# Performance work log

Measured on AMD Instinct MI355X. Metric: run time of the kernel, lower is better.

Reference implementation:

```python
import jax, jax.numpy as jnp
import numpy as np

BS, V, H, W = 2, 4, 24, 24
C, K, L, NH = 256, 16, 6, 8
DH = C // NH
FF = 4 * C
EPS = 1e-5


def _ln(x, w, b):
    m = jnp.mean(x, axis=-1, keepdims=True)
    v = jnp.mean((x - m) ** 2, axis=-1, keepdims=True)
    return (x - m) * jax.lax.rsqrt(v + EPS) * w + b


def _pe(x, W1, b1, W2, b2):
    # PositionEmbeddingLearnedMLP: Linear(3,C) -> ReLU -> Linear(C,C), channels-last
    return jax.nn.relu(x @ W1.T + b1) @ W2.T + b2


def setup_inputs():
    key = jax.random.key(0)
    ks = jax.random.split(key, 8)
    s = 0.02
    return {
        "feature": jax.random.normal(ks[0], (BS * V, C, H, W), jnp.float32),
        "xyz": jax.random.uniform(ks[1], (BS * V, H, W, 3), jnp.float32),
        "pe_W1": jax.random.normal(ks[2], (C, 3), jnp.float32) * s,
        "pe_b1": jnp.zeros((C,), jnp.float32),
        "pe_W2": jax.random.normal(ks[3], (C, C), jnp.float32) * s,
        "pe_b2": jnp.zeros((C,), jnp.float32),
        "Wqkv": jax.random.normal(ks[4], (L, 3 * C, C), jnp.float32) * s,
        "bqkv": jnp.zeros((L, 3 * C), jnp.float32),
        "Wo": jax.random.normal(ks[5], (L, C, C), jnp.float32) * s,
        "bo": jnp.zeros((L, C), jnp.float32),
        "ln_attn_w": jnp.ones((L, C), jnp.float32),
        "ln_attn_b": jnp.zeros((L, C), jnp.float32),
        "W1": jax.random.normal(ks[6], (L, FF, C), jnp.float32) * s,
        "b1": jnp.zeros((L, FF), jnp.float32),
        "W2": jax.random.normal(ks[7], (L, C, FF), jnp.float32) * s,
        "b2": jnp.zeros((L, C), jnp.float32),
        "ln_ffn_w": jnp.ones((L, C), jnp.float32),
        "ln_ffn_b": jnp.zeros((L, C), jnp.float32),
        "ln_out_w": jnp.ones((L, C), jnp.float32),
        "ln_out_b": jnp.zeros((L, C), jnp.float32),
    }


def _forward(feature, xyz, pe_W1, pe_b1, pe_W2, pe_b2, Wqkv, bqkv, Wo, bo,
             ln_attn_w, ln_attn_b, W1, b1, W2, b2, ln_ffn_w, ln_ffn_b,
             ln_out_w, ln_out_b):
    N = V * H * W
    # (B*V,C,H,W) -> (BS,N,C) ; (B*V,H,W,3) -> (BS,N,3) : flatten views+pixels
    feat = feature.reshape(BS, V, C, H, W).transpose(0, 1, 3, 4, 2).reshape(BS, N, C)
    pts = xyz.reshape(BS, N, 3)
    # per-batch KNN (self included), mirroring pointops.queryandgroup
    d2 = jnp.sum((pts[:, :, None, :] - pts[:, None, :, :]) ** 2, axis=-1)  # (BS,N,N)
    _, idx = jax.lax.top_k(-d2, K)  # (BS,N,K) nearest-neighbor indices
    grouped = jax.vmap(lambda p, i: p[i])(pts, idx)  # (BS,N,K,3)
    rel = grouped - pts[:, :, None, :]  # relative coords (use_xyz=True)
    q_pe = _pe(jnp.zeros((3,), feat.dtype), pe_W1, pe_b1, pe_W2, pe_b2)  # (C,)
    k_pe = _pe(rel, pe_W1, pe_b1, pe_W2, pe_b2).reshape(BS * N, K, C)
    idx_g = (idx + (jnp.arange(BS) * N)[:, None, None]).reshape(BS * N, K)
    out = feat.reshape(BS * N, C)
    for i in range(L):
        keyf = out[idx_g]  # (BN,K,C) per-layer neighbor gather
        # CrossAttentionLayer, pre-norm
        t2 = _ln(out, ln_attn_w[i], ln_attn_b[i])
        q = (t2 + q_pe) @ Wqkv[i, :C].T + bqkv[i, :C]
        k = (keyf + k_pe) @ Wqkv[i, C:2 * C].T + bqkv[i, C:2 * C]
        v = keyf @ Wqkv[i, 2 * C:].T + bqkv[i, 2 * C:]
        qh = q.reshape(-1, NH, DH)
        kh = k.reshape(-1, K, NH, DH)
        vh = v.reshape(-1, K, NH, DH)
        att = jax.nn.softmax(jnp.einsum('bhd,bkhd->bhk', qh, kh) * (DH ** -0.5), axis=-1)
        ao = jnp.einsum('bhk,bkhd->bhd', att, vh).reshape(-1, C) @ Wo[i].T + bo[i]
        out = out + ao
        # FFNLayer, pre-norm
        t2 = _ln(out, ln_ffn_w[i], ln_ffn_b[i])
        out = out + (jax.nn.relu(t2 @ W1[i].T + b1[i]) @ W2[i].T + b2[i])
        # extra per-layer LayerNorm
        out = _ln(out, ln_out_w[i], ln_out_b[i])
    return out.reshape(BS, V, H, W, C).transpose(0, 1, 4, 2, 3).reshape(BS * V, C, H, W)


def reference(feature, xyz, pe_W1, pe_b1, pe_W2, pe_b2, Wqkv, bqkv, Wo, bo,
              ln_attn_w, ln_attn_b, W1, b1, W2, b2, ln_ffn_w, ln_ffn_b,
              ln_out_w, ln_out_b):
    return _forward(feature, xyz, pe_W1, pe_b1, pe_W2, pe_b2, Wqkv, bqkv, Wo, bo,
                    ln_attn_w, ln_attn_b, W1, b1, W2, b2, ln_ffn_w, ln_ffn_b,
                    ln_out_w, ln_out_b)
```

## Files before the change

### kernel.cpp

```cpp
#include <hip/hip_runtime.h>
#include <math.h>

#define BS_ 2
#define V_ 4
#define H_ 24
#define W_ 24
#define N_ (V_*H_*W_)
#define BN_ (BS_*N_)
#define C_ 256
#define K_ 16
#define L_ 6
#define NH_ 8
#define DH_ 32
#define FF_ 1024

typedef __attribute__((ext_vector_type(4))) float f32x4;
typedef __attribute__((ext_vector_type(8))) short bf16x8;
typedef __attribute__((ext_vector_type(4))) unsigned u32x4;

__device__ inline unsigned short f2bf(float x) {
    unsigned u = __float_as_uint(x);
    unsigned r = u + 0x7fffu + ((u >> 16) & 1u);
    return (unsigned short)(r >> 16);
}
__device__ inline float bf2f(unsigned short h) {
    return __uint_as_float(((unsigned)h) << 16);
}

__global__ __launch_bounds__(256) void f2bf_kernel(const float* __restrict__ in,
                                                   unsigned short* __restrict__ out, int n) {
    int i = blockIdx.x*256 + threadIdx.x;
    if (i < n) out[i] = f2bf(in[i]);
}

__global__ __launch_bounds__(256) void w2frag_kernel(const float* __restrict__ W,
                                                     unsigned short* __restrict__ F,
                                                     int P, int K) {
    int wid = threadIdx.x >> 6, lane = threadIdx.x & 63;
    int tile = blockIdx.x*4 + wid;
    int nkt = K >> 5;
    int tn = tile / nkt, tk = tile - tn*nkt;
    const float* src = W + (size_t)(tn*16 + (lane & 15))*K + tk*32 + (lane >> 4)*8;
    unsigned short tmp[8];
    #pragma unroll
    for (int j = 0; j < 8; ++j) tmp[j] = f2bf(src[j]);
    *(bf16x8*)&F[(size_t)tile*512 + lane*8] = *(bf16x8*)tmp;
}

__global__ __launch_bounds__(256) void reshape_in_ln(const float* __restrict__ f,
                                                     const float* __restrict__ lnw,
                                                     const float* __restrict__ lnb,
                                                     const float* __restrict__ qpe,
                                                     float* __restrict__ w_out,
                                                     unsigned short* __restrict__ b_out,
                                                     unsigned short* __restrict__ b_t2) {
    int bn = blockIdx.x, c = threadIdx.x;
    int b = bn / N_, rem = bn % N_;
    int v = rem / (H_*W_), hw = rem % (H_*W_);
    float x = f[(((size_t)(b*V_ + v)*C_ + c)*(H_*W_)) + hw];
    w_out[(size_t)bn*C_ + c] = x;
    b_out[(size_t)bn*C_ + c] = f2bf(x);
    __shared__ float red[4];
    float s = x;
    #pragma unroll
    for (int off = 32; off; off >>= 1) s += __shfl_xor(s, off, 64);
    if ((c & 63) == 0) red[c >> 6] = s;
    __syncthreads();
    float mean = (red[0]+red[1]+red[2]+red[3]) * (1.f/C_);
    __syncthreads();
    float dx = x - mean;
    s = dx*dx;
    #pragma unroll
    for (int off = 32; off; off >>= 1) s += __shfl_xor(s, off, 64);
    if ((c & 63) == 0) red[c >> 6] = s;
    __syncthreads();
    float var = (red[0]+red[1]+red[2]+red[3]) * (1.f/C_);
    float y = dx * rsqrtf(var + 1e-5f) * lnw[c] + lnb[c] + qpe[c];
    b_t2[(size_t)bn*C_ + c] = f2bf(y);
}

__global__ __launch_bounds__(256) void reshape_out_kernel(const float* __restrict__ in,
                                                          float* __restrict__ o) {
    int bn = blockIdx.x, c = threadIdx.x;
    int b = bn / N_, rem = bn % N_;
    int v = rem / (H_*W_), hw = rem % (H_*W_);
    o[(((size_t)(b*V_ + v)*C_ + c)*(H_*W_)) + hw] = in[(size_t)bn*C_ + c];
}

__global__ __launch_bounds__(256) void knn_kernel(const float* __restrict__ pts,
                                                  int* __restrict__ idx) {
    int wid = threadIdx.x >> 6, lane = threadIdx.x & 63;
    int point = blockIdx.x*4 + wid;
    int b = point / N_;
    int il = point % N_;
    __shared__ float ps[N_*3];
    for (int l = threadIdx.x; l < N_*3; l += 256) ps[l] = pts[(size_t)b*N_*3 + l];
    __syncthreads();
    float qx = ps[il*3], qy = ps[il*3+1], qz = ps[il*3+2];
    unsigned long long key[36];
    #pragma unroll
    for (int s = 0; s < 36; ++s) {
        int j = lane + 64*s;
        float dx = qx - ps[j*3], dy = qy - ps[j*3+1], dz = qz - ps[j*3+2];
        float d2 = dx*dx + dy*dy + dz*dz;
        key[s] = ((unsigned long long)__float_as_uint(d2) << 32) | (unsigned)j;
    }
    for (int it = 0; it < K_; ++it) {
        unsigned long long b0 = key[0], b1 = key[1], b2 = key[2], b3 = key[3];
        #pragma unroll
        for (int s = 4; s < 36; s += 4) {
            b0 = key[s]   < b0 ? key[s]   : b0;
            b1 = key[s+1] < b1 ? key[s+1] : b1;
            b2 = key[s+2] < b2 ? key[s+2] : b2;
            b3 = key[s+3] < b3 ? key[s+3] : b3;
        }
        unsigned long long m01 = b0 < b1 ? b0 : b1;
        unsigned long long m23 = b2 < b3 ? b2 : b3;
        unsigned long long best = m01 < m23 ? m01 : m23;
        #pragma unroll
        for (int off = 32; off; off >>= 1) {
            unsigned long long o = __shfl_xor(best, off, 64);
            if (o < best) best = o;
        }
        int wj = (int)(best & 0xffffffffu);
        if (lane == 0) idx[point*K_ + it] = b*N_ + wj;
        if ((wj & 63) == lane) {
            int sw = wj >> 6;
            #pragma unroll
            for (int s = 0; s < 36; ++s) if (s == sw) key[s] = ~0ull;
        }
    }
}

__global__ __launch_bounds__(256) void qpe_kernel(const float* __restrict__ b1,
                                                  const float* __restrict__ W2,
                                                  const float* __restrict__ b2,
                                                  float* __restrict__ qpe) {
    __shared__ float h[C_];
    int tid = threadIdx.x;
    h[tid] = fmaxf(b1[tid], 0.f);
    __syncthreads();
    float acc = 0.f;
    for (int j = 0; j < C_; ++j) acc += h[j] * W2[(size_t)tid*C_ + j];
    qpe[tid] = acc + b2[tid];
}

__global__ __launch_bounds__(256) void pe_hidden_kernel(const float* __restrict__ pts,
                                                        const int* __restrict__ idx,
                                                        const float* __restrict__ W1,
                                                        const float* __restrict__ b1,
                                                        unsigned short* __restrict__ hidden) {
    int point = blockIdx.x;
    int c = threadIdx.x;
    __shared__ float rel[K_][3];
    if (threadIdx.x < K_*3) {
        int k = threadIdx.x / 3, ax = threadIdx.x % 3;
        int j = idx[point*K_ + k];
        rel[k][ax] = pts[(size_t)j*3 + ax] - pts[(size_t)point*3 + ax];
    }
    __syncthreads();
    float w0 = W1[c*3], w1 = W1[c*3+1], w2 = W1[c*3+2], bb = b1[c];
    #pragma unroll
    for (int k = 0; k < K_; ++k) {
        float v = rel[k][0]*w0 + rel[k][1]*w1 + rel[k][2]*w2 + bb;
        hidden[((size_t)point*K_ + k)*C_ + c] = f2bf(fmaxf(v, 0.f));
    }
}

template<int ACT, bool RES, int OMODE>
__device__ __forceinline__ void gemm_body2(const unsigned short* __restrict__ A, int sA,
                                           const unsigned short* __restrict__ Wf,
                                           const float* __restrict__ bias, int bcol0,
                                           const float* __restrict__ res,
                                           float* __restrict__ outF,
                                           unsigned short* __restrict__ outB,
                                           int sO, int on0, int m0, int K) {
    __shared__ unsigned short As[2][64][40];
    int tid = threadIdx.x;
    int wave = tid >> 6, lane = tid & 63;
    int wr = wave >> 1, wc = wave & 1;
    int nkt = K >> 5;
    f32x4 acc[2][2];
    #pragma unroll
    for (int i = 0; i < 2; ++i)
        #pragma unroll
        for (int j = 0; j < 2; ++j) acc[i][j] = (f32x4){0.f, 0.f, 0.f, 0.f};

    int r = tid >> 2, ch = tid & 3;
    const unsigned short* pA = A + (size_t)(m0 + r)*sA + ch*8;
    const unsigned short* bb = Wf + (size_t)(wc*2)*nkt*512 + lane*8;
    *(bf16x8*)&As[0][r][ch*8] = *(const bf16x8*)pA;
    bf16x8 bw0 = *(const bf16x8*)bb;
    bf16x8 bw1 = *(const bf16x8*)(bb + (size_t)nkt*512);
    __syncthreads();
    for (int t = 0; t < nkt; ++t) {
        int cur = t & 1;
        bool nx = (t + 1 < nkt);
        bf16x8 la, nb0, nb1;
        if (nx) {
            la  = *(const bf16x8*)(pA + (t+1)*32);
            nb0 = *(const bf16x8*)(bb + (size_t)(t+1)*512);
            nb1 = *(const bf16x8*)(bb + (size_t)nkt*512 + (size_t)(t+1)*512);
        }
        int kf = (lane >> 4) * 8;
        bf16x8 af0 = *(const bf16x8*)&As[cur][wr*32 + (lane & 15)][kf];
        bf16x8 af1 = *(const bf16x8*)&As[cur][wr*32 + 16 + (lane & 15)][kf];
        acc[0][0] = __builtin_amdgcn_mfma_f32_16x16x32_bf16(af0, bw0, acc[0][0], 0, 0, 0);
        acc[0][1] = __builtin_amdgcn_mfma_f32_16x16x32_bf16(af0, bw1, acc[0][1], 0, 0, 0);
        acc[1][0] = __builtin_amdgcn_mfma_f32_16x16x32_bf16(af1, bw0, acc[1][0], 0, 0, 0);
        acc[1][1] = __builtin_amdgcn_mfma_f32_16x16x32_bf16(af1, bw1, acc[1][1], 0, 0, 0);
        if (nx) *(bf16x8*)&As[cur^1][r][ch*8] = la;
        bw0 = nb0; bw1 = nb1;
        __syncthreads();
    }
    #pragma unroll
    for (int i = 0; i < 2; ++i) {
        #pragma unroll
        for (int j = 0; j < 2; ++j) {
            #pragma unroll
            for (int rg = 0; rg < 4; ++rg) {
                int m = m0 + wr*32 + i*16 + (lane >> 4)*4 + rg;
                int pl = wc*32 + j*16 + (lane & 15);
                float v = acc[i][j][rg];
                if (bias) v += bias[bcol0 + pl];
                if (ACT == 1) v = fmaxf(v, 0.f);
                if (RES) v += res[(size_t)m*sO + on0 + pl];
                if (OMODE != 2) outF[(size_t)m*sO + on0 + pl] = v;
                if (OMODE != 0) outB[(size_t)m*sO + on0 + pl] = f2bf(v);
            }
        }
    }
}

template<int ACT, bool RES, int OMODE>
__global__ __launch_bounds__(256) void gemm_k2(const unsigned short* __restrict__ A,
                                               const unsigned short* __restrict__ Wf0,
                                               const float* __restrict__ bias,
                                               const float* __restrict__ res,
                                               float* __restrict__ outF,
                                               unsigned short* __restrict__ outB,
                                               int P, int K) {
    int n0 = blockIdx.x * 64, m0 = blockIdx.y * 64;
    const unsigned short* Wf = Wf0 + (size_t)(n0 >> 4)*(K >> 5)*512;
    gemm_body2<ACT,RES,OMODE>(A, K, Wf, bias, n0, res, outF, outB, P, n0, m0, K);
}

__global__ __launch_bounds__(256) void qkv_kernel2(const unsigned short* __restrict__ t2,
                                                   const unsigned short* __restrict__ outb,
                                                   const unsigned short* __restrict__ Fqkv_l,
                                                   const float* __restrict__ bqkv_l,
                                                   unsigned short* __restrict__ b_q,
                                                   unsigned short* __restrict__ b_kv) {
    int bx = blockIdx.x;
    int m0 = blockIdx.y * 64;
    const unsigned short* Wf = Fqkv_l + (size_t)(bx*4)*8*512;
    if (bx < 4) {
        gemm_body2<0,false,2>(t2, C_, Wf, bqkv_l, bx*64, nullptr, nullptr, b_q, 256, bx*64, m0, C_);
    } else {
        gemm_body2<0,false,2>(outb, C_, Wf, bqkv_l, bx*64, nullptr, nullptr, b_kv, 512, bx*64 - 256, m0, C_);
    }
}

template<int VAR>
__global__ __launch_bounds__(256) void gemm_ln2(const unsigned short* __restrict__ A,
                                                const unsigned short* __restrict__ Wf,
                                                const float* __restrict__ bias,
                                                const float* __restrict__ res,
                                                const float* __restrict__ lnw1, const float* __restrict__ lnb1,
                                                const float* __restrict__ lnw2, const float* __restrict__ lnb2,
                                                const float* __restrict__ qpe,
                                                float* __restrict__ outF,
                                                unsigned short* __restrict__ outB,
                                                unsigned short* __restrict__ outT2,
                                                int K) {
    __shared__ unsigned short As[2][16][40];
    __shared__ float S[16][260];
    int tid = threadIdx.x;
    int wave = tid >> 6, lane = tid & 63;
    int m0 = blockIdx.x * 16;
    int nkt = K >> 5;
    f32x4 acc[4];
    #pragma unroll
    for (int j = 0; j < 4; ++j) acc[j] = (f32x4){0.f,0.f,0.f,0.f};
    const unsigned short* pA = A + (size_t)(m0 + ((tid & 63) >> 2))*K + (tid & 3)*8;
    const unsigned short* bb = Wf + (size_t)(wave*4)*nkt*512 + lane*8;
    if (tid < 64) *(bf16x8*)&As[0][tid >> 2][(tid & 3)*8] = *(const bf16x8*)pA;
    bf16x8 bw[4];
    #pragma unroll
    for (int j = 0; j < 4; ++j) bw[j] = *(const bf16x8*)(bb + (size_t)j*nkt*512);
    __syncthreads();
    for (int t = 0; t < nkt; ++t) {
        int cur = t & 1;
        bool nx = (t + 1 < nkt);
        bf16x8 la, nb0, nb1, nb2, nb3;
        if (nx) {
            nb0 = *(const bf16x8*)(bb + (size_t)0*nkt*512 + (size_t)(t+1)*512);
            nb1 = *(const bf16x8*)(bb + (size_t)1*nkt*512 + (size_t)(t+1)*512);
            nb2 = *(const bf16x8*)(bb + (size_t)2*nkt*512 + (size_t)(t+1)*512);
            nb3 = *(const bf16x8*)(bb + (size_t)3*nkt*512 + (size_t)(t+1)*512);
            if (tid < 64) la = *(const bf16x8*)(pA + (t+1)*32);
        }
        int kf = (lane >> 4) * 8;
        bf16x8 af = *(const bf16x8*)&As[cur][lane & 15][kf];
        acc[0] = __builtin_amdgcn_mfma_f32_16x16x32_bf16(af, bw[0], acc[0], 0, 0, 0);
        acc[1] = __builtin_amdgcn_mfma_f32_16x16x32_bf16(af, bw[1], acc[1], 0, 0, 0);
        acc[2] = __builtin_amdgcn_mfma_f32_16x16x32_bf16(af, bw[2], acc[2], 0, 0, 0);
        acc[3] = __builtin_amdgcn_mfma_f32_16x16x32_bf16(af, bw[3], acc[3], 0, 0, 0);
        if (nx) {
            if (tid < 64) *(bf16x8*)&As[cur^1][tid >> 2][(tid & 3)*8] = la;
            bw[0] = nb0; bw[1] = nb1; bw[2] = nb2; bw[3] = nb3;
        }
        __syncthreads();
    }
    #pragma unroll
    for (int j = 0; j < 4; ++j) {
        int col = wave*64 + j*16 + (lane & 15);
        #pragma unroll
        for (int rg = 0; rg < 4; ++rg) {
            int row = (lane >> 4)*4 + rg;
            S[row][col] = acc[j][rg] + bias[col] + res[(size_t)(m0+row)*C_ + col];
        }
    }
    __syncthreads();
    int row = tid >> 4, g = tid & 15;
    size_t m = m0 + row;
    float x[16];
    #pragma unroll
    for (int u = 0; u < 4; ++u) {
        f32x4 v4 = *(const f32x4*)&S[row][g*16 + u*4];
        x[u*4+0] = v4[0]; x[u*4+1] = v4[1]; x[u*4+2] = v4[2]; x[u*4+3] = v4[3];
    }
    float s1 = 0.f, s2 = 0.f;
    #pragma unroll
    for (int u = 0; u < 16; ++u) { s1 += x[u]; s2 += x[u]*x[u]; }
    #pragma unroll
    for (int off = 8; off; off >>= 1) { s1 += __shfl_xor(s1, off, 16); s2 += __shfl_xor(s2, off, 16); }
    float mean = s1 * (1.f/C_);
    float var  = s2 * (1.f/C_) - mean*mean;
    float rstd = rsqrtf(var + 1e-5f);
    float y1[16];
    #pragma unroll
    for (int u = 0; u < 4; ++u) {
        f32x4 w4 = *(const f32x4*)&lnw1[g*16 + u*4];
        f32x4 b4 = *(const f32x4*)&lnb1[g*16 + u*4];
        #pragma unroll
        for (int v = 0; v < 4; ++v)
            y1[u*4+v] = (x[u*4+v] - mean)*rstd*w4[v] + b4[v];
    }
    if (VAR == 0) {
        #pragma unroll
        for (int u = 0; u < 4; ++u) {
            f32x4 v4 = { x[u*4], x[u*4+1], x[u*4+2], x[u*4+3] };
            *(f32x4*)&outF[m*C_ + g*16 + u*4] = v4;
        }
        unsigned pk[8];
        #pragma unroll
        for (int u = 0; u < 8; ++u) pk[u] = (unsigned)f2bf(y1[2*u]) | ((unsigned)f2bf(y1[2*u+1]) << 16);
        *(u32x4*)&outT2[m*C_ + g*16]     = *(u32x4*)&pk[0];
        *(u32x4*)&outT2[m*C_ + g*16 + 8] = *(u32x4*)&pk[4];
    } else {
        #pragma unroll
        for (int u = 0; u < 4; ++u) {
            f32x4 v4 = { y1[u*4], y1[u*4+1], y1[u*4+2], y1[u*4+3] };
            *(f32x4*)&outF[m*C_ + g*16 + u*4] = v4;
        }
        if (VAR == 1) {
            unsigned pk[8];
            #pragma unroll
            for (int u = 0; u < 8; ++u) pk[u] = (unsigned)f2bf(y1[2*u]) | ((unsigned)f2bf(y1[2*u+1]) << 16);
            *(u32x4*)&outB[m*C_ + g*16]     = *(u32x4*)&pk[0];
            *(u32x4*)&outB[m*C_ + g*16 + 8] = *(u32x4*)&pk[4];
            float t1 = 0.f, t2s = 0.f;
            #pragma unroll
            for (int u = 0; u < 16; ++u) { t1 += y1[u]; t2s += y1[u]*y1[u]; }
            #pragma unroll
            for (int off = 8; off; off >>= 1) { t1 += __shfl_xor(t1, off, 16); t2s += __shfl_xor(t2s, off, 16); }
            float mean2 = t1 * (1.f/C_);
            float var2  = t2s * (1.f/C_) - mean2*mean2;
            float rstd2 = rsqrtf(var2 + 1e-5f);
            unsigned pk2[8];
            #pragma unroll
            for (int u = 0; u < 4; ++u) {
                f32x4 w4 = *(const f32x4*)&lnw2[g*16 + u*4];
                f32x4 b4 = *(const f32x4*)&lnb2[g*16 + u*4];
                f32x4 q4 = *(const f32x4*)&qpe[g*16 + u*4];
                float z0 = (y1[u*4+0]-mean2)*rstd2*w4[0] + b4[0] + q4[0];
                float z1 = (y1[u*4+1]-mean2)*rstd2*w4[1] + b4[1] + q4[1];
                float z2 = (y1[u*4+2]-mean2)*rstd2*w4[2] + b4[2] + q4[2];
                float z3 = (y1[u*4+3]-mean2)*rstd2*w4[3] + b4[3] + q4[3];
                pk2[u*2]   = (unsigned)f2bf(z0) | ((unsigned)f2bf(z1) << 16);
                pk2[u*2+1] = (unsigned)f2bf(z2) | ((unsigned)f2bf(z3) << 16);
            }
            *(u32x4*)&outT2[m*C_ + g*16]     = *(u32x4*)&pk2[0];
            *(u32x4*)&outT2[m*C_ + g*16 + 8] = *(u32x4*)&pk2[4];
        }
    }
}

__global__ __launch_bounds__(256) void rk_kernel(const unsigned short* __restrict__ q,
                                                 const unsigned short* __restrict__ Wqkv_l,
                                                 unsigned short* __restrict__ r) {
    int n0 = blockIdx.x * 64, m0 = blockIdx.y * 64, h = blockIdx.z;
    __shared__ unsigned short As[64][40];
    __shared__ unsigned short Ws[64][40];
    int tid = threadIdx.x;
    int wave = tid >> 6, lane = tid & 63;
    int wr = wave >> 1, wc = wave & 1;
    *(bf16x8*)&As[tid>>2][(tid&3)*8] =
        *(const bf16x8*)&q[(size_t)(m0 + (tid>>2))*C_ + h*DH_ + (tid&3)*8];
    {
        int d = tid >> 3, cg = tid & 7;
        bf16x8 wv = *(const bf16x8*)&Wqkv_l[(size_t)(C_ + h*DH_ + d)*C_ + n0 + cg*8];
        #pragma unroll
        for (int j = 0; j < 8; ++j) Ws[cg*8 + j][d] = (unsigned short)wv[j];
    }
    __syncthreads();
    int kf = (lane >> 4) * 8;
    bf16x8 af[2], wf[2];
    #pragma unroll
    for (int i = 0; i < 2; ++i) af[i] = *(const bf16x8*)&As[wr*32 + i*16 + (lane & 15)][kf];
    #pragma unroll
    for (int j = 0; j < 2; ++j) wf[j] = *(const bf16x8*)&Ws[wc*32 + j*16 + (lane & 15)][kf];
    f32x4 acc[2][2];
    #pragma unroll
    for (int i = 0; i < 2; ++i)
        #pragma unroll
        for (int j = 0; j < 2; ++j)
            acc[i][j] = __builtin_amdgcn_mfma_f32_16x16x32_bf16(af[i], wf[j],
                          (f32x4){0.f,0.f,0.f,0.f}, 0, 0, 0);
    #pragma unroll
    for (int i = 0; i < 2; ++i)
        #pragma unroll
        for (int j = 0; j < 2; ++j)
            #pragma unroll
            for (int rg = 0; rg < 4; ++rg) {
                int m = m0 + wr*32 + i*16 + (lane >> 4)*4 + rg;
                int pl = wc*32 + j*16 + (lane & 15);
                r[(size_t)m*(NH_*C_) + h*C_ + n0 + pl] = f2bf(acc[i][j][rg]);
            }
}

__global__ __launch_bounds__(256) void attn_kernel(const unsigned short* __restrict__ q,
                                                   const unsigned short* __restrict__ kv,
                                                   const unsigned short* __restrict__ kpe,
                                                   const unsigned short* __restrict__ r,
                                                   const int* __restrict__ idx,
                                                   unsigned short* __restrict__ ao) {
    int wid = threadIdx.x >> 6, lane = threadIdx.x & 63;
    int point = blockIdx.x*4 + wid;
    __shared__ __align__(16) unsigned short vs[4][K_][264];
    __shared__ __align__(16) float atts[4][NH_][K_];
    int row = lane & 15;
    int off8 = (lane >> 4) * 8;
    int idx_l = idx[point*K_ + row];

    #pragma unroll
    for (int t = 0; t < 8; ++t) {
        int vr = 2*t + (lane >> 5);
        int j = __shfl(idx_l, vr, 64);
        int cc = (lane & 31) * 8;
        *(bf16x8*)&vs[wid][vr][cc] = *(const bf16x8*)&kv[(size_t)j*512 + 256 + cc];
    }

    f32x4 acc = {0.f, 0.f, 0.f, 0.f};
    const bf16x8 zero8 = {0,0,0,0,0,0,0,0};
    #pragma unroll
    for (int s = 0; s < 8; ++s) {
        bf16x8 a = *(const bf16x8*)&kpe[((size_t)point*K_ + row)*C_ + s*32 + off8];
        bf16x8 b = zero8;
        if (row < 8) b = *(const bf16x8*)&r[(size_t)point*NH_*C_ + row*C_ + s*32 + off8];
        acc = __builtin_amdgcn_mfma_f32_16x16x32_bf16(a, b, acc, 0, 0, 0);
    }
    #pragma unroll
    for (int s = 0; s < 8; ++s) {
        bf16x8 a = *(const bf16x8*)&kv[(size_t)idx_l*512 + s*32 + off8];
        bf16x8 b = zero8;
        if (row == 8 + s) b = *(const bf16x8*)&q[(size_t)point*C_ + s*32 + off8];
        acc = __builtin_amdgcn_mfma_f32_16x16x32_bf16(a, b, acc, 0, 0, 0);
    }

    const float scale = 0.1767766952966369f;
    float sv[4], m = -1e30f;
    #pragma unroll
    for (int rg = 0; rg < 4; ++rg) {
        float o = __shfl_xor(acc[rg], 8, 64);
        sv[rg] = (acc[rg] + o) * scale;
        m = fmaxf(m, sv[rg]);
    }
    m = fmaxf(m, __shfl_xor(m, 16, 64));
    m = fmaxf(m, __shfl_xor(m, 32, 64));
    float sum = 0.f;
    #pragma unroll
    for (int rg = 0; rg < 4; ++rg) { sv[rg] = __expf(sv[rg] - m); sum += sv[rg]; }
    sum += __shfl_xor(sum, 16, 64);
    sum += __shfl_xor(sum, 32, 64);
    float inv = 1.f / sum;
    if (row < 8) {
        f32x4 av = { sv[0]*inv, sv[1]*inv, sv[2]*inv, sv[3]*inv };
        *(f32x4*)&atts[wid][row][(lane >> 4) * 4] = av;
    }

    int h = lane >> 3;
    float att_f[16];
    #pragma unroll
    for (int u = 0; u < 4; ++u) {
        f32x4 t4 = *(const f32x4*)&atts[wid][h][u*4];
        att_f[u*4+0] = t4[0]; att_f[u*4+1] = t4[1]; att_f[u*4+2] = t4[2]; att_f[u*4+3] = t4[3];
    }
    int cbase = lane * 4;
    float o0 = 0.f, o1 = 0.f, o2 = 0.f, o3 = 0.f;
    #pragma unroll
    for (int k = 0; k < K_; ++k) {
        unsigned long long vv = *(const unsigned long long*)&vs[wid][k][cbase];
        unsigned lo = (unsigned)vv, hi = (unsigned)(vv >> 32);
        float a = att_f[k];
        o0 += a * __uint_as_float(lo << 16);
        o1 += a * __uint_as_float(lo & 0xffff0000u);
        o2 += a * __uint_as_float(hi << 16);
        o3 += a * __uint_as_float(hi & 0xffff0000u);
    }
    unsigned p0 = (unsigned)f2bf(o0) | ((unsigned)f2bf(o1) << 16);
    unsigned p1 = (unsigned)f2bf(o2) | ((unsigned)f2bf(o3) << 16);
    unsigned out2[2] = { p0, p1 };
    *(unsigned long long*)&ao[(size_t)point*C_ + cbase] = *(const unsigned long long*)out2;
}

extern "C" void kernel_launch(void* const* d_in, const int* in_sizes, int n_in,
                              void* d_out, int out_size, void* d_ws, size_t ws_size,
                              hipStream_t stream) {
    const float* feature  = (const float*)d_in[0];
    const float* xyz      = (const float*)d_in[1];
    const float* pe_W1    = (const float*)d_in[2];
    const float* pe_b1    = (const float*)d_in[3];
    const float* pe_W2    = (const float*)d_in[4];
    const float* pe_b2    = (const float*)d_in[5];
    const float* Wqkv     = (const float*)d_in[6];
    const float* bqkv     = (const float*)d_in[7];
    const float* Wo       = (const float*)d_in[8];
    const float* bo       = (const float*)d_in[9];
    const float* ln_attn_w= (const float*)d_in[10];
    const float* ln_attn_b= (const float*)d_in[11];
    const float* W1       = (const float*)d_in[12];
    const float* b1       = (const float*)d_in[13];
    const float* W2       = (const float*)d_in[14];
    const float* b2       = (const float*)d_in[15];
    const float* ln_ffn_w = (const float*)d_in[16];
    const float* ln_ffn_b = (const float*)d_in[17];
    const float* ln_out_w = (const float*)d_in[18];
    const float* ln_out_b = (const float*)d_in[19];

    float* ws = (float*)d_ws;
    float* w_out = ws;
    float* w_qpe = w_out + (size_t)BN_*C_;
    unsigned short* bptr = (unsigned short*)(w_qpe + C_ + 64);
    unsigned short* b_out = bptr;  bptr += (size_t)BN_*C_;
    unsigned short* b_t2  = bptr;  bptr += (size_t)BN_*C_;
    unsigned short* b_q   = bptr;  bptr += (size_t)BN_*C_;
    unsigned short* b_kv  = bptr;  bptr += (size_t)BN_*512;
    unsigned short* b_ao  = bptr;  bptr += (size_t)BN_*C_;
    unsigned short* b_ffh = bptr;  bptr += (size_t)BN_*FF_;
    unsigned short* w_kpe = bptr;  bptr += (size_t)BN_*K_*C_;
    unsigned short* w_r   = bptr;  bptr += (size_t)BN_*NH_*C_;
    unsigned short* b_hid = bptr;  bptr += (size_t)BN_*K_*C_;
    unsigned short* bWqkv = bptr;  bptr += (size_t)L_*3*C_*C_;
    unsigned short* Fqkv  = bptr;  bptr += (size_t)L_*3*C_*C_;
    unsigned short* Fo    = bptr;  bptr += (size_t)L_*C_*C_;
    unsigned short* F1    = bptr;  bptr += (size_t)L_*FF_*C_;
    unsigned short* F2    = bptr;  bptr += (size_t)L_*C_*FF_;
    unsigned short* Fpe   = bptr;  bptr += (size_t)C_*C_;
    int* w_idx = (int*)bptr;

    f2bf_kernel<<<(L_*3*C_*C_+255)/256, 256, 0, stream>>>(Wqkv, bWqkv, L_*3*C_*C_);
    w2frag_kernel<<<(L_*3*C_*C_/512)/4, 256, 0, stream>>>(Wqkv, Fqkv, L_*3*C_, C_);
    w2frag_kernel<<<(L_*C_*C_/512)/4,   256, 0, stream>>>(Wo,   Fo,   L_*C_,   C_);
    w2frag_kernel<<<(L_*FF_*C_/512)/4,  256, 0, stream>>>(W1,   F1,   L_*FF_,  C_);
    w2frag_kernel<<<(L_*C_*FF_/512)/4,  256, 0, stream>>>(W2,   F2,   L_*C_,   FF_);
    w2frag_kernel<<<(C_*C_/512)/4,      256, 0, stream>>>(pe_W2, Fpe, C_,      C_);

    knn_kernel<<<BN_/4, 256, 0, stream>>>(xyz, w_idx);
    qpe_kernel<<<1, 256, 0, stream>>>(pe_b1, pe_W2, pe_b2, w_qpe);
    reshape_in_ln<<<BN_, 256, 0, stream>>>(feature, ln_attn_w, ln_attn_b, w_qpe,
                                           w_out, b_out, b_t2);
    pe_hidden_kernel<<<BN_, 256, 0, stream>>>(xyz, w_idx, pe_W1, pe_b1, b_hid);
    gemm_k2<0,false,2><<<dim3(C_/64, (BN_*K_)/64), 256, 0, stream>>>(
        b_hid, Fpe, pe_b2, nullptr, nullptr, w_kpe, C_, C_);

    for (int i = 0; i < L_; ++i) {
        const unsigned short* Fqkv_l = Fqkv + (size_t)i*3*C_*C_;
        const float* bqkv_l = bqkv + (size_t)i*3*C_;

        qkv_kernel2<<<dim3(12, BN_/64), 256, 0, stream>>>(b_t2, b_out, Fqkv_l, bqkv_l, b_q, b_kv);
        rk_kernel<<<dim3(4, BN_/64, NH_), 256, 0, stream>>>(b_q, bWqkv + (size_t)i*3*C_*C_, w_r);
        attn_kernel<<<BN_/4, 256, 0, stream>>>(b_q, b_kv, w_kpe, w_r, w_idx, b_ao);
        gemm_ln2<0><<<BN_/16, 256, 0, stream>>>(
            b_ao, Fo + (size_t)i*C_*C_, bo + i*C_, w_out,
            ln_ffn_w + i*C_, ln_ffn_b + i*C_, nullptr, nullptr, nullptr,
            w_out, nullptr, b_t2, C_);
        gemm_k2<1,false,2><<<dim3(FF_/64, BN_/64), 256, 0, stream>>>(
            b_t2, F1 + (size_t)i*FF_*C_, b1 + i*FF_, nullptr, nullptr, b_ffh, FF_, C_);
        if (i < L_-1) {
            gemm_ln2<1><<<BN_/16, 256, 0, stream>>>(
                b_ffh, F2 + (size_t)i*C_*FF_, b2 + i*C_, w_out,
                ln_out_w + i*C_, ln_out_b + i*C_,
                ln_attn_w + (i+1)*C_, ln_attn_b + (i+1)*C_, w_qpe,
                w_out, b_out, b_t2, FF_);
        } else {
            gemm_ln2<2><<<BN_/16, 256, 0, stream>>>(
                b_ffh, F2 + (size_t)i*C_*FF_, b2 + i*C_, w_out,
                ln_out_w + i*C_, ln_out_b + i*C_, nullptr, nullptr, nullptr,
                w_out, nullptr, nullptr, FF_);
        }
    }

    reshape_out_kernel<<<BN_, 256, 0, stream>>>(w_out, (float*)d_out);
}
```

Before: 666.7 us.

## Fuse FFN up-projection, ReLU, down-projection and LayerNorm into one kernel

Replaces the separate FF1 GEMM and the FF2+LayerNorm kernel with a single ffn_ln kernel. Each block handles 16 rows: it computes the 1024-wide ReLU hidden activations into shared memory, then runs the down-projection and the shared LN epilogue. This removes the global round trip for the hidden buffer and one launch per layer. In exchange, weight fragments are read directly from global memory without LDS staging or prefetching, and every 16-row block rereads the full W1 and W2. The kernel also uses about 60KB of shared memory, which may limit occupancy.

```diff
diff --git a/kernel.cpp b/kernel.cpp
--- a/kernel.cpp
+++ b/kernel.cpp
@@ -258,6 +258,90 @@
         gemm_body2<0,false,2>(t2, C_, Wf, bqkv_l, bx*64, nullptr, nullptr, b_q, 256, bx*64, m0, C_);
     } else {
         gemm_body2<0,false,2>(outb, C_, Wf, bqkv_l, bx*64, nullptr, nullptr, b_kv, 512, bx*64 - 256, m0, C_);
+    }
+}
+
+template<int VAR>
+__device__ __forceinline__ void ln_epilogue(float (*S)[260], int m0,
+                                            const float* __restrict__ lnw1, const float* __restrict__ lnb1,
+                                            const float* __restrict__ lnw2, const float* __restrict__ lnb2,
+                                            const float* __restrict__ qpe,
+                                            float* __restrict__ outF,
+                                            unsigned short* __restrict__ outB,
+                                            unsigned short* __restrict__ outT2) {
+    int tid = threadIdx.x;
+    int row = tid >> 4, g = tid & 15;
+    size_t m = m0 + row;
+    float x[16];
+    #pragma unroll
+    for (int u = 0; u < 4; ++u) {
+        f32x4 v4 = *(const f32x4*)&S[row][g*16 + u*4];
+        x[u*4+0] = v4[0]; x[u*4+1] = v4[1]; x[u*4+2] = v4[2]; x[u*4+3] = v4[3];
+    }
+    float s1 = 0.f, s2 = 0.f;
+    #pragma unroll
+    for (int u = 0; u < 16; ++u) { s1 += x[u]; s2 += x[u]*x[u]; }
+    #pragma unroll
+    for (int off = 8; off; off >>= 1) { s1 += __shfl_xor(s1, off, 16); s2 += __shfl_xor(s2, off, 16); }
+    float mean = s1 * (1.f/C_);
+    float var  = s2 * (1.f/C_) - mean*mean;
+    float rstd = rsqrtf(var + 1e-5f);
+    float y1[16];
+    #pragma unroll
+    for (int u = 0; u < 4; ++u) {
+        f32x4 w4 = *(const f32x4*)&lnw1[g*16 + u*4];
+        f32x4 b4 = *(const f32x4*)&lnb1[g*16 + u*4];
+        #pragma unroll
+        for (int v = 0; v < 4; ++v)
+            y1[u*4+v] = (x[u*4+v] - mean)*rstd*w4[v] + b4[v];
+    }
+    if (VAR == 0) {
+        #pragma unroll
+        for (int u = 0; u < 4; ++u) {
+            f32x4 v4 = { x[u*4], x[u*4+1], x[u*4+2], x[u*4+3] };
+            *(f32x4*)&outF[m*C_ + g*16 + u*4] = v4;
+        }
+        unsigned pk[8];
+        #pragma unroll
+        for (int u = 0; u < 8; ++u) pk[u] = (unsigned)f2bf(y1[2*u]) | ((unsigned)f2bf(y1[2*u+1]) << 16);
+        *(u32x4*)&outT2[m*C_ + g*16]     = *(u32x4*)&pk[0];
+        *(u32x4*)&outT2[m*C_ + g*16 + 8] = *(u32x4*)&pk[4];
+    } else {
+        #pragma unroll
+        for (int u = 0; u < 4; ++u) {
+            f32x4 v4 = { y1[u*4], y1[u*4+1], y1[u*4+2], y1[u*4+3] };
+            *(f32x4*)&outF[m*C_ + g*16 + u*4] = v4;
+        }
+        if (VAR == 1) {
+            unsigned pk[8];
+            #pragma unroll
+            for (int u = 0; u < 8; ++u) pk[u] = (unsigned)f2bf(y1[2*u]) | ((unsigned)f2bf(y1[2*u+1]) << 16);
+            *(u32x4*)&outB[m*C_ + g*16]     = *(u32x4*)&pk[0];
+            *(u32x4*)&outB[m*C_ + g*16 + 8] = *(u32x4*)&pk[4];
+            float t1 = 0.f, t2s = 0.f;
+            #pragma unroll
+            for (int u = 0; u < 16; ++u) { t1 += y1[u]; t2s += y1[u]*y1[u]; }
+            #pragma unroll
+            for (int off = 8; off; off >>= 1) { t1 += __shfl_xor(t1, off, 16); t2s += __shfl_xor(t2s, off, 16); }
+            float mean2 = t1 * (1.f/C_);
+            float var2  = t2s * (1.f/C_) - mean2*mean2;
+            float rstd2 = rsqrtf(var2 + 1e-5f);
+            unsigned pk2[8];
+            #pragma unroll
+            for (int u = 0; u < 4; ++u) {
+                f32x4 w4 = *(const f32x4*)&lnw2[g*16 + u*4];
+                f32x4 b4 = *(const f32x4*)&lnb2[g*16 + u*4];
+                f32x4 q4 = *(const f32x4*)&qpe[g*16 + u*4];
+                float z0 = (y1[u*4+0]-mean2)*rstd2*w4[0] + b4[0] + q4[0];
+                float z1 = (y1[u*4+1]-mean2)*rstd2*w4[1] + b4[1] + q4[1];
+                float z2 = (y1[u*4+2]-mean2)*rstd2*w4[2] + b4[2] + q4[2];
+                float z3 = (y1[u*4+3]-mean2)*rstd2*w4[3] + b4[3] + q4[3];
+                pk2[u*2]   = (unsigned)f2bf(z0) | ((unsigned)f2bf(z1) << 16);
+                pk2[u*2+1] = (unsigned)f2bf(z2) | ((unsigned)f2bf(z3) << 16);
+            }
+            *(u32x4*)&outT2[m*C_ + g*16]     = *(u32x4*)&pk2[0];
+            *(u32x4*)&outT2[m*C_ + g*16 + 8] = *(u32x4*)&pk2[4];
+        }
     }
 }
 
@@ -322,79 +406,88 @@
         }
     }
     __syncthreads();
-    int row = tid >> 4, g = tid & 15;
-    size_t m = m0 + row;
-    float x[16];
-    #pragma unroll
-    for (int u = 0; u < 4; ++u) {
-        f32x4 v4 = *(const f32x4*)&S[row][g*16 + u*4];
-        x[u*4+0] = v4[0]; x[u*4+1] = v4[1]; x[u*4+2] = v4[2]; x[u*4+3] = v4[3];
-    }
-    float s1 = 0.f, s2 = 0.f;
-    #pragma unroll
-    for (int u = 0; u < 16; ++u) { s1 += x[u]; s2 += x[u]*x[u]; }
-    #pragma unroll
-    for (int off = 8; off; off >>= 1) { s1 += __shfl_xor(s1, off, 16); s2 += __shfl_xor(s2, off, 16); }
-    float mean = s1 * (1.f/C_);
-    float var  = s2 * (1.f/C_) - mean*mean;
-    float rstd = rsqrtf(var + 1e-5f);
-    float y1[16];
-    #pragma unroll
-    for (int u = 0; u < 4; ++u) {
-        f32x4 w4 = *(const f32x4*)&lnw1[g*16 + u*4];
-        f32x4 b4 = *(const f32x4*)&lnb1[g*16 + u*4];
-        #pragma unroll
-        for (int v = 0; v < 4; ++v)
-            y1[u*4+v] = (x[u*4+v] - mean)*rstd*w4[v] + b4[v];
-    }
-    if (VAR == 0) {
-        #pragma unroll
-        for (int u = 0; u < 4; ++u) {
-            f32x4 v4 = { x[u*4], x[u*4+1], x[u*4+2], x[u*4+3] };
-            *(f32x4*)&outF[m*C_ + g*16 + u*4] = v4;
-        }
-        unsigned pk[8];
-        #pragma unroll
-        for (int u = 0; u < 8; ++u) pk[u] = (unsigned)f2bf(y1[2*u]) | ((unsigned)f2bf(y1[2*u+1]) << 16);
-        *(u32x4*)&outT2[m*C_ + g*16]     = *(u32x4*)&pk[0];
-        *(u32x4*)&outT2[m*C_ + g*16 + 8] = *(u32x4*)&pk[4];
-    } else {
-        #pragma unroll
-        for (int u = 0; u < 4; ++u) {
-            f32x4 v4 = { y1[u*4], y1[u*4+1], y1[u*4+2], y1[u*4+3] };
-            *(f32x4*)&outF[m*C_ + g*16 + u*4] = v4;
-        }
-        if (VAR == 1) {
-            unsigned pk[8];
-            #pragma unroll
-            for (int u = 0; u < 8; ++u) pk[u] = (unsigned)f2bf(y1[2*u]) | ((unsigned)f2bf(y1[2*u+1]) << 16);
-            *(u32x4*)&outB[m*C_ + g*16]     = *(u32x4*)&pk[0];
-            *(u32x4*)&outB[m*C_ + g*16 + 8] = *(u32x4*)&pk[4];
-            float t1 = 0.f, t2s = 0.f;
-            #pragma unroll
-            for (int u = 0; u < 16; ++u) { t1 += y1[u]; t2s += y1[u]*y1[u]; }
-            #pragma unroll
-            for (int off = 8; off; off >>= 1) { t1 += __shfl_xor(t1, off, 16); t2s += __shfl_xor(t2s, off, 16); }
-            float mean2 = t1 * (1.f/C_);
-            float var2  = t2s * (1.f/C_) - mean2*mean2;
-            float rstd2 = rsqrtf(var2 + 1e-5f);
-            unsigned pk2[8];
-            #pragma unroll
-            for (int u = 0; u < 4; ++u) {
-                f32x4 w4 = *(const f32x4*)&lnw2[g*16 + u*4];
-                f32x4 b4 = *(const f32x4*)&lnb2[g*16 + u*4];
-                f32x4 q4 = *(const f32x4*)&qpe[g*16 + u*4];
-                float z0 = (y1[u*4+0]-mean2)*rstd2*w4[0] + b4[0] + q4[0];
-                float z1 = (y1[u*4+1]-mean2)*rstd2*w4[1] + b4[1] + q4[1];
-                float z2 = (y1[u*4+2]-mean2)*rstd2*w4[2] + b4[2] + q4[2];
-                float z3 = (y1[u*4+3]-mean2)*rstd2*w4[3] + b4[3] + q4[3];
-                pk2[u*2]   = (unsigned)f2bf(z0) | ((unsigned)f2bf(z1) << 16);
-                pk2[u*2+1] = (unsigned)f2bf(z2) | ((unsigned)f2bf(z3) << 16);
+    ln_epilogue<VAR>(S, m0, lnw1, lnb1, lnw2, lnb2, qpe, outF, outB, outT2);
+}
+
+template<int VAR>
+__global__ __launch_bounds__(256) void ffn_ln(const unsigned short* __restrict__ t2,
+                                              const unsigned short* __restrict__ F1,
+                                              const float* __restrict__ b1v,
+                                              const unsigned short* __restrict__ F2,
+                                              const float* __restrict__ b2v,
+                                              const float* __restrict__ res,
+                                              const float* __restrict__ lnw1, const float* __restrict__ lnb1,
+                                              const float* __restrict__ lnw2, const float* __restrict__ lnb2,
+                                              const float* __restrict__ qpe,
+                                              float* __restrict__ outF,
+                                              unsigned short* __restrict__ outB,
+                                              unsigned short* __restrict__ outT2) {
+    __shared__ unsigned short tS[16][264];
+    __shared__ unsigned short hS[16][1032];
+    __shared__ float S[16][260];
+    int tid = threadIdx.x;
+    int wave = tid >> 6, lane = tid & 63;
+    int m0 = blockIdx.x * 16;
+    int kf = (lane >> 4) * 8;
+
+    #pragma unroll
+    for (int u = 0; u < 2; ++u) {
+        int id = tid + u*256;
+        int rr = id >> 5, cc = id & 31;
+        *(bf16x8*)&tS[rr][cc*8] = *(const bf16x8*)&t2[(size_t)(m0+rr)*C_ + cc*8];
+    }
+    __syncthreads();
+
+    for (int nc = 0; nc < 4; ++nc) {
+        f32x4 acc[4];
+        #pragma unroll
+        for (int j = 0; j < 4; ++j) acc[j] = (f32x4){0.f,0.f,0.f,0.f};
+        const unsigned short* bb = F1 + ((size_t)(nc*16 + wave*4)*8)*512 + lane*8;
+        #pragma unroll
+        for (int t = 0; t < 8; ++t) {
+            bf16x8 af = *(const bf16x8*)&tS[lane & 15][t*32 + kf];
+            #pragma unroll
+            for (int j = 0; j < 4; ++j) {
+                bf16x8 wf = *(const bf16x8*)(bb + ((size_t)j*8 + t)*512);
+                acc[j] = __builtin_amdgcn_mfma_f32_16x16x32_bf16(af, wf, acc[j], 0, 0, 0);
             }
-            *(u32x4*)&outT2[m*C_ + g*16]     = *(u32x4*)&pk2[0];
-            *(u32x4*)&outT2[m*C_ + g*16 + 8] = *(u32x4*)&pk2[4];
-        }
-    }
+        }
+        #pragma unroll
+        for (int j = 0; j < 4; ++j) {
+            int col = nc*256 + wave*64 + j*16 + (lane & 15);
+            float bc = b1v[col];
+            #pragma unroll
+            for (int rg = 0; rg < 4; ++rg) {
+                int row = (lane >> 4)*4 + rg;
+                hS[row][col] = f2bf(fmaxf(acc[j][rg] + bc, 0.f));
+            }
+        }
+    }
+    __syncthreads();
+
+    f32x4 acc2[4];
+    #pragma unroll
+    for (int j = 0; j < 4; ++j) acc2[j] = (f32x4){0.f,0.f,0.f,0.f};
+    const unsigned short* bb2 = F2 + ((size_t)(wave*4)*32)*512 + lane*8;
+    for (int t = 0; t < 32; ++t) {
+        bf16x8 af = *(const bf16x8*)&hS[lane & 15][t*32 + kf];
+        #pragma unroll
+        for (int j = 0; j < 4; ++j) {
+            bf16x8 wf = *(const bf16x8*)(bb2 + ((size_t)j*32 + t)*512);
+            acc2[j] = __builtin_amdgcn_mfma_f32_16x16x32_bf16(af, wf, acc2[j], 0, 0, 0);
+        }
+    }
+    #pragma unroll
+    for (int j = 0; j < 4; ++j) {
+        int col = wave*64 + j*16 + (lane & 15);
+        #pragma unroll
+        for (int rg = 0; rg < 4; ++rg) {
+            int row = (lane >> 4)*4 + rg;
+            S[row][col] = acc2[j][rg] + b2v[col] + res[(size_t)(m0+row)*C_ + col];
+        }
+    }
+    __syncthreads();
+    ln_epilogue<VAR>(S, m0, lnw1, lnb1, lnw2, lnb2, qpe, outF, outB, outT2);
 }
 
 __global__ __launch_bounds__(256) void rk_kernel(const unsigned short* __restrict__ q,
@@ -558,7 +651,6 @@
     unsigned short* b_q   = bptr;  bptr += (size_t)BN_*C_;
     unsigned short* b_kv  = bptr;  bptr += (size_t)BN_*512;
     unsigned short* b_ao  = bptr;  bptr += (size_t)BN_*C_;
-    unsigned short* b_ffh = bptr;  bptr += (size_t)BN_*FF_;
     unsigned short* w_kpe = bptr;  bptr += (size_t)BN_*K_*C_;
     unsigned short* w_r   = bptr;  bptr += (size_t)BN_*NH_*C_;
     unsigned short* b_hid = bptr;  bptr += (size_t)BN_*K_*C_;
@@ -596,19 +688,19 @@
             b_ao, Fo + (size_t)i*C_*C_, bo + i*C_, w_out,
             ln_ffn_w + i*C_, ln_ffn_b + i*C_, nullptr, nullptr, nullptr,
             w_out, nullptr, b_t2, C_);
-        gemm_k2<1,false,2><<<dim3(FF_/64, BN_/64), 256, 0, stream>>>(
-            b_t2, F1 + (size_t)i*FF_*C_, b1 + i*FF_, nullptr, nullptr, b_ffh, FF_, C_);
         if (i < L_-1) {
-            gemm_ln2<1><<<BN_/16, 256, 0, stream>>>(
-                b_ffh, F2 + (size_t)i*C_*FF_, b2 + i*C_, w_out,
+            ffn_ln<1><<<BN_/16, 256, 0, stream>>>(
+                b_t2, F1 + (size_t)i*FF_*C_, b1 + i*FF_,
+                F2 + (size_t)i*C_*FF_, b2 + i*C_, w_out,
                 ln_out_w + i*C_, ln_out_b + i*C_,
                 ln_attn_w + (i+1)*C_, ln_attn_b + (i+1)*C_, w_qpe,
-                w_out, b_out, b_t2, FF_);
+                w_out, b_out, b_t2);
         } else {
-            gemm_ln2<2><<<BN_/16, 256, 0, stream>>>(
-                b_ffh, F2 + (size_t)i*C_*FF_, b2 + i*C_, w_out,
+            ffn_ln<2><<<BN_/16, 256, 0, stream>>>(
+                b_t2, F1 + (size_t)i*FF_*C_, b1 + i*FF_,
+                F2 + (size_t)i*C_*FF_, b2 + i*C_, w_out,
                 ln_out_w + i*C_, ln_out_b + i*C_, nullptr, nullptr, nullptr,
-                w_out, nullptr, nullptr, FF_);
+                w_out, nullptr, nullptr);
         }
     }
 
```

Result: faster. 599.1 us, median of 2 (-10.1%).
